# Kernel tuning notes

Measured on AMD Instinct MI355X. Metric: run time of the kernel, lower is better.

The kernel has to match this reference:

```python
import jax, jax.numpy as jnp
import numpy as np

N = 20000      # nodes
E = 320000     # edges (avg degree 16)
C = 64         # channels per degree
H = 8          # attention heads
DIM1 = 3       # degree-1 representation dim (2*1+1)
NUM_FEATURES = C * 1 + C * 3  # key_fiber.num_features = 256


def setup_inputs() -> dict:
    key = jax.random.key(0)
    ks = jax.random.split(key, 7)
    return {
        "value_0": jax.random.normal(ks[0], (E, C, 1), dtype=jnp.float32),
        "value_1": jax.random.normal(ks[1], (E, C, DIM1), dtype=jnp.float32),
        "key_0": jax.random.normal(ks[2], (E, C, 1), dtype=jnp.float32),
        "key_1": jax.random.normal(ks[3], (E, C, DIM1), dtype=jnp.float32),
        "query_0": jax.random.normal(ks[4], (N, C, 1), dtype=jnp.float32),
        "query_1": jax.random.normal(ks[5], (N, C, DIM1), dtype=jnp.float32),
        "dst": jax.random.randint(ks[6], (E,), 0, N),
    }


def _to_heads(f0, f1):
    # Fiber.to_attention_heads: per degree [n, C, dim] -> [n, H, (C//H)*dim], concat on last dim
    n = f0.shape[0]
    return jnp.concatenate([f0.reshape(n, H, -1), f1.reshape(n, H, -1)], axis=-1)


def reference(value_0, value_1, key_0, key_1, query_0, query_1, dst):
    k = _to_heads(key_0, key_1)        # [E, H, Dk]
    q = _to_heads(query_0, query_1)    # [N, H, Dk]
    # dgl.ops.e_dot_v: dot edge key with destination-node query, then scale
    logits = jnp.einsum('ehd,ehd->eh', k, q[dst]) / np.float32(np.sqrt(NUM_FEATURES))
    edge_prelogits = logits            # returned pre-softmax (scaled) as in original
    # edge_softmax over incoming edges of each destination node, per head
    m = jax.ops.segment_max(logits, dst, num_segments=N)           # [N, H]
    w = jnp.exp(logits - m[dst])                                   # [E, H]
    denom = jax.ops.segment_sum(w, dst, num_segments=N)            # [N, H]
    alpha = w / denom[dst]                                         # [E, H]

    def agg(v, dim):
        # value view: [E, H, C//H, dim]; weighted copy_e_sum -> [N, C, dim]
        vh = v.reshape(E, H, C // H, dim)
        out = jax.ops.segment_sum(alpha[:, :, None, None] * vh, dst, num_segments=N)
        return out.reshape(N, C, dim)

    out_0 = agg(value_0, 1)
    out_1 = agg(value_1, DIM1)
    return out_0, out_1, edge_prelogits
```

## Files before the change

kernel.cpp:

```cpp
#include <hip/hip_runtime.h>

#define N_NODES 20000
#define N_EDGES 320000
#define SLOTS  48


#define DOT4(a,b) ((a).x*(b).x + (a).y*(b).y + (a).z*(b).z + (a).w*(b).w)
#define FMA4(a,s,p) { (a).x += (s)*(p).x; (a).y += (s)*(p).y; (a).z += (s)*(p).z; (a).w += (s)*(p).w; }
#define RED4(a,m) { (a).x += __shfl_xor((a).x,m); (a).y += __shfl_xor((a).y,m); \
                    (a).z += __shfl_xor((a).z,m); (a).w += __shfl_xor((a).w,m); }

__global__ __launch_bounds__(256) void k_zero(int* __restrict__ p, int n)
{
    int i = blockIdx.x * 256 + threadIdx.x;
    if (i < n) p[i] = 0;
}

__global__ __launch_bounds__(256) void k_fill(
    const int* __restrict__ dst, int* __restrict__ counts, int* __restrict__ bucket)
{
    int e = blockIdx.x * 256 + threadIdx.x;
    if (e >= N_EDGES) return;
    int d = dst[e];
    int cnt = atomicAdd(&counts[d], 1);
    if (cnt < SLOTS) bucket[d * SLOTS + cnt] = e;
}


#define LOADR(R, E, A0, A1, A2, A3)                                             \
{                                                                               \
    int g = base + s2 + 4 * (R);                                                \
    int idx = min(g, dm1);                                                      \
    E = bucket[bb + idx];                                                       \
    const float4* kr0 = (const float4*)(k0 + (size_t)E * 64);                   \
    const float4* kr1 = (const float4*)(k1 + (size_t)E * 192);                  \
    A0 = kr0[c]; A1 = kr1[c]; A2 = kr1[c + 16]; A3 = kr1[c + 32];               \
}

__global__ __launch_bounds__(256) void k_logits(
    const float* __restrict__ k0, const float* __restrict__ k1,
    const float* __restrict__ q0, const float* __restrict__ q1,
    const int* __restrict__ counts, const int* __restrict__ bucket,
    float* __restrict__ logits, float* __restrict__ Rtab)
{
    __shared__ float4 part4[4 * 256];
    int w = threadIdx.x >> 6, l = threadIdx.x & 63;
    int node = blockIdx.x * 4 + w;
    int deg = min(counts[node], SLOTS);
    int bb = node * SLOTS;
    int dm1 = (deg > 0) ? deg - 1 : 0;

    int s2 = l >> 4, c = l & 15;
    int sl = l >> 3, h = l & 7;

    const float4* q0f = (const float4*)(q0 + (size_t)node * 64);
    const float4* q1f = (const float4*)(q1 + (size_t)node * 192);
    float4 Q0 = q0f[c], Q1a = q1f[c], Q1b = q1f[c + 16], Q1c = q1f[c + 32];

    float* pf = (float*)part4 + (size_t)w * 1024;
    int ro[8];
    ro[0] = (2 * h) * 4 + 0;
    ro[1] = (2 * h + 1) * 4 + 0;
#pragma unroll
    for (int kk = 0; kk < 6; ++kk) {
        int i = 6 * h + kk;
        ro[2 + kk] = (i & 15) * 4 + 1 + (i >> 4);
    }

    float S = 0.f;

#pragma unroll
    for (int pass = 0; pass < 3; ++pass) {
        int base = pass * 16;
        bool act = base < deg;

        if (act) {
            int e0, e1, e2, e3;
            float4 A00, A01, A02, A03, A10, A11, A12, A13;
            float4 A20, A21, A22, A23, A30, A31, A32, A33;
            LOADR(0, e0, A00, A01, A02, A03)
            LOADR(1, e1, A10, A11, A12, A13)
            LOADR(2, e2, A20, A21, A22, A23)
            LOADR(3, e3, A30, A31, A32, A33)
            float4* wp = part4 + w * 256;
            wp[(s2     ) * 16 + c] = make_float4(DOT4(A00,Q0), DOT4(A01,Q1a), DOT4(A02,Q1b), DOT4(A03,Q1c));
            wp[(s2 +  4) * 16 + c] = make_float4(DOT4(A10,Q0), DOT4(A11,Q1a), DOT4(A12,Q1b), DOT4(A13,Q1c));
            wp[(s2 +  8) * 16 + c] = make_float4(DOT4(A20,Q0), DOT4(A21,Q1a), DOT4(A22,Q1b), DOT4(A23,Q1c));
            wp[(s2 + 12) * 16 + c] = make_float4(DOT4(A30,Q0), DOT4(A31,Q1a), DOT4(A32,Q1b), DOT4(A33,Q1c));
        }
        __syncthreads();
        if (act) {
#pragma unroll
            for (int m = 0; m < 2; ++m) {
                int srow = sl + 8 * m;
                int slot = base + srow;
                if (slot < deg) {
                    const float* row = pf + srow * 64;
                    float x = row[ro[0]] + row[ro[1]] + row[ro[2]] + row[ro[3]]
                            + row[ro[4]] + row[ro[5]] + row[ro[6]] + row[ro[7]];
                    x *= 0.0625f;
                    int e = bucket[bb + slot];
                    logits[(size_t)e * 8 + h] = x;
                    S += __expf(x);
                }
            }
        }
        __syncthreads();
    }

    S += __shfl_xor(S, 8);
    S += __shfl_xor(S, 16);
    S += __shfl_xor(S, 32);
    if (l < 8 && deg > 0) Rtab[node * 8 + l] = 1.f / S;
}

#define B_BODY(BASE)                                                            \
{                                                                               \
    int sA = (BASE) + s2, sB = (BASE) + s2 + 4;                                 \
    int eA = bucket[bb + min(sA, deg - 1)];                                     \
    int eB = bucket[bb + min(sB, deg - 1)];                                     \
    const float* lrA = logits + (size_t)eA * 8;                                 \
    const float* lrB = logits + (size_t)eB * 8;                                 \
    float xA0 = lrA[hv0], xAa = lrA[hv1a], xAb = lrA[hv1b], xAc = lrA[hv1c];    \
    float xB0 = lrB[hv0], xBa = lrB[hv1a], xBb = lrB[hv1b], xBc = lrB[hv1c];    \
    const float4* r0A = (const float4*)(v0 + (size_t)eA * 64);                  \
    const float4* r1A = (const float4*)(v1 + (size_t)eA * 192);                 \
    const float4* r0B = (const float4*)(v0 + (size_t)eB * 64);                  \
    const float4* r1B = (const float4*)(v1 + (size_t)eB * 192);                 \
    float4 P0A = r0A[c], PaA = r1A[c], PbA = r1A[c + 16], PcA = r1A[c + 32];    \
    float4 P0B = r0B[c], PaB = r1B[c], PbB = r1B[c + 16], PcB = r1B[c + 32];    \
    float wA0 = __expf(xA0) * R0, wAa = __expf(xAa) * Ra;                       \
    float wAb = __expf(xAb) * Rb, wAc = __expf(xAc) * Rc;                       \
    float wB0 = __expf(xB0) * R0, wBa = __expf(xBa) * Ra;                       \
    float wBb = __expf(xBb) * Rb, wBc = __expf(xBc) * Rc;                       \
    if (sA >= deg) { wA0 = wAa = wAb = wAc = 0.f; }                             \
    if (sB >= deg) { wB0 = wBa = wBb = wBc = 0.f; }                             \
    FMA4(a0, wA0, P0A); FMA4(a1a, wAa, PaA); FMA4(a1b, wAb, PbA); FMA4(a1c, wAc, PcA); \
    FMA4(a0, wB0, P0B); FMA4(a1a, wBa, PaB); FMA4(a1b, wBb, PbB); FMA4(a1c, wBc, PcB); \
}

__global__ __launch_bounds__(256) void k_agg(
    const float* __restrict__ v0, const float* __restrict__ v1,
    const float* __restrict__ logits, const int* __restrict__ counts,
    const int* __restrict__ bucket, const float* __restrict__ Rtab,
    float* __restrict__ out0, float* __restrict__ out1)
{
    int w = threadIdx.x >> 6, l = threadIdx.x & 63;
    int node = blockIdx.x * 4 + w;
    int deg = min(counts[node], SLOTS);
    int bb = node * SLOTS;
    int s2 = l >> 4, c = l & 15;

    if (deg == 0) {
        if (l < 16) {
            float4 z = {0,0,0,0};
            ((float4*)(out0 + (size_t)node * 64))[c] = z;
            float4* o1 = (float4*)(out1 + (size_t)node * 192);
            o1[c] = z; o1[c + 16] = z; o1[c + 32] = z;
        }
        return;
    }

    int hv0  = c >> 1;
    int hv1a = c / 6;
    int hv1b = (c + 16) / 6;
    int hv1c = (c + 32) / 6;
    float R0 = Rtab[node * 8 + hv0];
    float Ra = Rtab[node * 8 + hv1a];
    float Rb = Rtab[node * 8 + hv1b];
    float Rc = Rtab[node * 8 + hv1c];

    float4 a0 = {0,0,0,0}, a1a = {0,0,0,0}, a1b = {0,0,0,0}, a1c = {0,0,0,0};

    B_BODY(0)
    if (deg > 8)  B_BODY(8)
    if (deg > 16) B_BODY(16)
    if (deg > 24) B_BODY(24)
    if (deg > 32) B_BODY(32)
    if (deg > 40) B_BODY(40)

    RED4(a0, 16);  RED4(a0, 32);
    RED4(a1a, 16); RED4(a1a, 32);
    RED4(a1b, 16); RED4(a1b, 32);
    RED4(a1c, 16); RED4(a1c, 32);

    if (l < 16) {
        float4* o0 = (float4*)(out0 + (size_t)node * 64);
        float4* o1 = (float4*)(out1 + (size_t)node * 192);
        o0[c]      = a0;
        o1[c]      = a1a;
        o1[c + 16] = a1b;
        o1[c + 32] = a1c;
    }
}

extern "C" void kernel_launch(void* const* d_in, const int* in_sizes, int n_in,
                              void* d_out, int out_size, void* d_ws, size_t ws_size,
                              hipStream_t stream) {
    const float* v0 = (const float*)d_in[0];
    const float* v1 = (const float*)d_in[1];
    const float* k0 = (const float*)d_in[2];
    const float* k1 = (const float*)d_in[3];
    const float* q0 = (const float*)d_in[4];
    const float* q1 = (const float*)d_in[5];
    const int*  dst = (const int*)d_in[6];

    float* out0   = (float*)d_out;
    float* out1   = out0 + (size_t)N_NODES * 64;
    float* logits = out1 + (size_t)N_NODES * 192;

    int*   wsI    = (int*)d_ws;
    int*   counts = wsI;
    int*   bucket = wsI + 20000;
    float* Rtab   = (float*)(wsI + 980000);

    k_zero   <<<79,   256, 0, stream>>>(counts, N_NODES);
    k_fill   <<<1250, 256, 0, stream>>>(dst, counts, bucket);
    k_logits <<<5000, 256, 0, stream>>>(k0, k1, q0, q1, counts, bucket,
                                        logits, Rtab);
    k_agg    <<<5000, 256, 0, stream>>>(v0, v1, logits, counts, bucket, Rtab,
                                        out0, out1);
}
```

Measured before the change: 191.2 us.

## Issue all edge key loads upfront and reduce logits after a single barrier

Restructures the logits kernel so each wave issues every key-row gather for up to 48 edges before any reduction, instead of three load/sync/reduce passes. Partial dot products go into a larger LDS buffer with rows padded to 17 float4 to avoid bank conflicts. The reduction then runs once after a single barrier. The aim is more memory-level parallelism and fewer barriers, at the cost of more registers and more LDS per block, which may lower occupancy.

```diff
diff --git a/kernel.cpp b/kernel.cpp
--- a/kernel.cpp
+++ b/kernel.cpp
@@ -27,14 +27,15 @@
 }
 
 
-#define LOADR(R, E, A0, A1, A2, A3)                                             \
+#define PLOAD(R, PR)                                                            \
 {                                                                               \
-    int g = base + s2 + 4 * (R);                                                \
-    int idx = min(g, dm1);                                                      \
-    E = bucket[bb + idx];                                                       \
+    int slot = 4 * (R) + s2;                                                    \
+    int idx = min(slot, dm1);                                                   \
+    int E = bucket[bb + idx];                                                   \
     const float4* kr0 = (const float4*)(k0 + (size_t)E * 64);                   \
     const float4* kr1 = (const float4*)(k1 + (size_t)E * 192);                  \
-    A0 = kr0[c]; A1 = kr1[c]; A2 = kr1[c + 16]; A3 = kr1[c + 32];               \
+    float4 A0 = kr0[c], A1 = kr1[c], A2 = kr1[c + 16], A3 = kr1[c + 32];        \
+    PR = make_float4(DOT4(A0, Q0), DOT4(A1, Q1a), DOT4(A2, Q1b), DOT4(A3, Q1c));\
 }
 
 __global__ __launch_bounds__(256) void k_logits(
@@ -43,7 +44,7 @@
     const int* __restrict__ counts, const int* __restrict__ bucket,
     float* __restrict__ logits, float* __restrict__ Rtab)
 {
-    __shared__ float4 part4[4 * 256];
+    __shared__ float4 lds[4 * SLOTS * 17];
     int w = threadIdx.x >> 6, l = threadIdx.x & 63;
     int node = blockIdx.x * 4 + w;
     int deg = min(counts[node], SLOTS);
@@ -57,10 +58,43 @@
     const float4* q1f = (const float4*)(q1 + (size_t)node * 192);
     float4 Q0 = q0f[c], Q1a = q1f[c], Q1b = q1f[c + 16], Q1c = q1f[c + 32];
 
-    float* pf = (float*)part4 + (size_t)w * 1024;
+    float4 p0, p1, p2, p3, p4, p5, p6, p7, p8, p9, p10, p11;
+    p0 = p1 = p2 = p3 = p4 = p5 = p6 = p7 = p8 = p9 = p10 = p11
+       = make_float4(0.f, 0.f, 0.f, 0.f);
+    if (deg > 0) {
+        PLOAD(0, p0)
+        PLOAD(1, p1)
+        PLOAD(2, p2)
+        PLOAD(3, p3)
+        if (deg > 16) { PLOAD(4, p4) PLOAD(5, p5) PLOAD(6, p6) PLOAD(7, p7) }
+        if (deg > 32) { PLOAD(8, p8) PLOAD(9, p9) PLOAD(10, p10) PLOAD(11, p11) }
+    }
+
+    float4* wp = lds + w * (SLOTS * 17);
+    if (deg > 0) {
+        wp[(0 * 4 + s2) * 17 + c] = p0;
+        wp[(1 * 4 + s2) * 17 + c] = p1;
+        wp[(2 * 4 + s2) * 17 + c] = p2;
+        wp[(3 * 4 + s2) * 17 + c] = p3;
+        if (deg > 16) {
+            wp[(4 * 4 + s2) * 17 + c] = p4;
+            wp[(5 * 4 + s2) * 17 + c] = p5;
+            wp[(6 * 4 + s2) * 17 + c] = p6;
+            wp[(7 * 4 + s2) * 17 + c] = p7;
+        }
+        if (deg > 32) {
+            wp[(8 * 4 + s2) * 17 + c]  = p8;
+            wp[(9 * 4 + s2) * 17 + c]  = p9;
+            wp[(10 * 4 + s2) * 17 + c] = p10;
+            wp[(11 * 4 + s2) * 17 + c] = p11;
+        }
+    }
+    __syncthreads();
+
+    const float* pf = (const float*)wp;
     int ro[8];
-    ro[0] = (2 * h) * 4 + 0;
-    ro[1] = (2 * h + 1) * 4 + 0;
+    ro[0] = (2 * h) * 4;
+    ro[1] = (2 * h + 1) * 4;
 #pragma unroll
     for (int kk = 0; kk < 6; ++kk) {
         int i = 6 * h + kk;
@@ -68,44 +102,18 @@
     }
 
     float S = 0.f;
-
 #pragma unroll
-    for (int pass = 0; pass < 3; ++pass) {
-        int base = pass * 16;
-        bool act = base < deg;
-
-        if (act) {
-            int e0, e1, e2, e3;
-            float4 A00, A01, A02, A03, A10, A11, A12, A13;
-            float4 A20, A21, A22, A23, A30, A31, A32, A33;
-            LOADR(0, e0, A00, A01, A02, A03)
-            LOADR(1, e1, A10, A11, A12, A13)
-            LOADR(2, e2, A20, A21, A22, A23)
-            LOADR(3, e3, A30, A31, A32, A33)
-            float4* wp = part4 + w * 256;
-            wp[(s2     ) * 16 + c] = make_float4(DOT4(A00,Q0), DOT4(A01,Q1a), DOT4(A02,Q1b), DOT4(A03,Q1c));
-            wp[(s2 +  4) * 16 + c] = make_float4(DOT4(A10,Q0), DOT4(A11,Q1a), DOT4(A12,Q1b), DOT4(A13,Q1c));
-            wp[(s2 +  8) * 16 + c] = make_float4(DOT4(A20,Q0), DOT4(A21,Q1a), DOT4(A22,Q1b), DOT4(A23,Q1c));
-            wp[(s2 + 12) * 16 + c] = make_float4(DOT4(A30,Q0), DOT4(A31,Q1a), DOT4(A32,Q1b), DOT4(A33,Q1c));
-        }
-        __syncthreads();
-        if (act) {
-#pragma unroll
-            for (int m = 0; m < 2; ++m) {
-                int srow = sl + 8 * m;
-                int slot = base + srow;
-                if (slot < deg) {
-                    const float* row = pf + srow * 64;
-                    float x = row[ro[0]] + row[ro[1]] + row[ro[2]] + row[ro[3]]
-                            + row[ro[4]] + row[ro[5]] + row[ro[6]] + row[ro[7]];
-                    x *= 0.0625f;
-                    int e = bucket[bb + slot];
-                    logits[(size_t)e * 8 + h] = x;
-                    S += __expf(x);
-                }
-            }
-        }
-        __syncthreads();
+    for (int m = 0; m < 6; ++m) {
+        int slot = sl + 8 * m;
+        if (slot < deg) {
+            const float* row = pf + slot * 68;
+            float x = row[ro[0]] + row[ro[1]] + row[ro[2]] + row[ro[3]]
+                    + row[ro[4]] + row[ro[5]] + row[ro[6]] + row[ro[7]];
+            x *= 0.0625f;
+            int e = bucket[bb + slot];
+            logits[(size_t)e * 8 + h] = x;
+            S += __expf(x);
+        }
     }
 
     S += __shfl_xor(S, 8);
```

After: 190.2 us. No clear change (-0.5%).
